# Kernel optimization log

Hardware: AMD Instinct MI355X
Metric: run time of the kernel (lower is better)

Reference implementation:

```python
import jax, jax.numpy as jnp
import numpy as np

# BigBird-roberta-base config with block_size=64, 12 layers
B = 1; S = 2048; D = 768; F = 3072; V = 50358
L = 12; H = 12; HD = 64; BS = 64; NB = S // BS; R = 3
NEG = -1.0e9
NKB = 5 + R           # global(2) + window(3) + random(3) key blocks per query block
NK = NKB * BS         # gathered keys per query block


def _block_map(nb, r, seed=0):
    """Static per-query-block key-block indices + dedup mask (first occurrence kept)."""
    rng = np.random.default_rng(seed)
    idx = np.zeros((nb, 5 + r), np.int32)
    dedup = np.ones((nb, 5 + r), np.float32)
    for i in range(nb):
        lst = [0, nb - 1, max(i - 1, 0), i, min(i + 1, nb - 1)]
        cand = np.setdiff1d(np.arange(nb), np.array(lst))
        lst += list(rng.choice(cand, r, replace=False))
        seen = set()
        for j, b in enumerate(lst):
            idx[i, j] = int(b)
            if b in seen:
                dedup[i, j] = 0.0
            seen.add(int(b))
    return idx, dedup

BLK_IDX, BLK_DEDUP = _block_map(NB, R)


def layer_norm(x, s, b):
    m = jnp.mean(x, axis=-1, keepdims=True)
    v = jnp.mean(jnp.square(x - m), axis=-1, keepdims=True)
    return (x - m) * jax.lax.rsqrt(v + 1e-12) * s + b


def bigbird_attn(x, wq, wk, wv, bq, bk, bv, wo, bo, key_mask):
    # x: [B,S,D]; key_mask: [B,S] float (1=keep)
    q = (x @ wq + bq).reshape(B, S, H, HD).transpose(0, 2, 1, 3)  # [B,H,S,HD]
    k = (x @ wk + bk).reshape(B, S, H, HD).transpose(0, 2, 1, 3)
    v = (x @ wv + bv).reshape(B, S, H, HD).transpose(0, 2, 1, 3)
    scale = 1.0 / np.sqrt(HD)
    qb = q.reshape(B, H, NB, BS, HD)
    kb = k.reshape(B, H, NB, BS, HD)
    vb = v.reshape(B, H, NB, BS, HD)
    # gather sparse key/value blocks: [B,H,NB,NKB,BS,HD] -> [B,H,NB,NK,HD]
    kg = kb[:, :, BLK_IDX].reshape(B, H, NB, NK, HD)
    vg = vb[:, :, BLK_IDX].reshape(B, H, NB, NK, HD)
    scores = jnp.einsum('bhnqd,bhnkd->bhnqk', qb, kg) * scale  # [B,H,NB,BS,NK]
    kmb = key_mask.reshape(B, NB, BS)[:, BLK_IDX]               # [B,NB,NKB,BS]
    m = (kmb * BLK_DEDUP[None, :, :, None]).reshape(B, 1, NB, 1, NK)
    probs = jax.nn.softmax(scores + (1.0 - m) * NEG, axis=-1)
    ctx = jnp.einsum('bhnqk,bhnkd->bhnqd', probs, vg)           # [B,H,NB,BS,HD]
    # global query blocks (first & last) attend densely to all keys
    qg = jnp.concatenate([qb[:, :, 0], qb[:, :, -1]], axis=2)   # [B,H,2*BS,HD]
    sg = jnp.einsum('bhqd,bhkd->bhqk', qg, k) * scale
    sg = sg + (1.0 - key_mask[:, None, None, :]) * NEG
    cg = jnp.einsum('bhqk,bhkd->bhqd', jax.nn.softmax(sg, axis=-1), v)
    ctx = ctx.at[:, :, 0].set(cg[:, :, :BS]).at[:, :, -1].set(cg[:, :, BS:])
    ctx = ctx.reshape(B, H, S, HD).transpose(0, 2, 1, 3).reshape(B, S, D)
    return ctx @ wo + bo


def setup_inputs() -> dict:
    key = jax.random.key(0)
    ks = jax.random.split(key, 16)
    p = lambda k, shape: jax.random.normal(k, shape, jnp.float32) * 0.02
    return {
        'input_ids': jax.random.randint(ks[0], (B, S), 0, V),
        'attention_mask': jnp.ones((B, S), jnp.int32),
        'token_type_ids': jnp.zeros((B, S), jnp.int32),
        'word_emb': p(ks[1], (V, D)),
        'pos_emb': p(ks[2], (S, D)),
        'type_emb': p(ks[3], (2, D)),
        'emb_ln_s': jnp.ones((D,)), 'emb_ln_b': jnp.zeros((D,)),
        'Wq': p(ks[4], (L, D, D)), 'Wk': p(ks[5], (L, D, D)), 'Wv': p(ks[6], (L, D, D)),
        'bq': jnp.zeros((L, D)), 'bk': jnp.zeros((L, D)), 'bv': jnp.zeros((L, D)),
        'Wo': p(ks[7], (L, D, D)), 'bo': jnp.zeros((L, D)),
        'ln1_s': jnp.ones((L, D)), 'ln1_b': jnp.zeros((L, D)),
        'W1': p(ks[8], (L, D, F)), 'b1': jnp.zeros((L, F)),
        'W2': p(ks[9], (L, F, D)), 'b2': jnp.zeros((L, D)),
        'ln2_s': jnp.ones((L, D)), 'ln2_b': jnp.zeros((L, D)),
        'fc_w': p(ks[10], (D, V)), 'fc_b': jnp.zeros((V,)),
    }


def reference(input_ids, attention_mask, token_type_ids, word_emb, pos_emb, type_emb,
              emb_ln_s, emb_ln_b, Wq, Wk, Wv, bq, bk, bv, Wo, bo, ln1_s, ln1_b,
              W1, b1, W2, b2, ln2_s, ln2_b, fc_w, fc_b):
    x = word_emb[input_ids] + pos_emb[None] + type_emb[token_type_ids]
    x = layer_norm(x, emb_ln_s, emb_ln_b)
    km = attention_mask.astype(x.dtype)
    for l in range(L):
        a = bigbird_attn(x, Wq[l], Wk[l], Wv[l], bq[l], bk[l], bv[l], Wo[l], bo[l], km)
        x = layer_norm(x + a, ln1_s[l], ln1_b[l])
        hdd = jax.nn.gelu(x @ W1[l] + b1[l])
        x = layer_norm(x + hdd @ W2[l] + b2[l], ln2_s[l], ln2_b[l])
    return x @ fc_w + fc_b  # logits [B,S,V]
```

## Files before the change

kernel.cpp:

```cpp
#include <hip/hip_runtime.h>
#include <hip/hip_bf16.h>


#define S_LEN 2048
#define DMODEL 768
#define FFDIM 3072
#define VOCAB 50358
#define VPAD  50432
#define NLAYER 12
#define NHEAD 12
#define NB 32
#define NKB 8
#define QKVN 2304

typedef __attribute__((ext_vector_type(8))) short bfrag8;
typedef __attribute__((ext_vector_type(8))) unsigned short us8;
typedef __attribute__((ext_vector_type(4))) float facc4;

__device__ __forceinline__ unsigned short f2bf(float f) {
  unsigned int u = __builtin_bit_cast(unsigned int, f);
  u += 0x7fffu + ((u >> 16) & 1u);
  return (unsigned short)(u >> 16);
}
__device__ __forceinline__ float bf2f(unsigned short h) {
  unsigned int u = ((unsigned int)h) << 16;
  return __builtin_bit_cast(float, u);
}

#define MFMA16(a, b, c) __builtin_amdgcn_mfma_f32_16x16x32_bf16((a), (b), (c), 0, 0, 0)
#define GLDS16(g, l) __builtin_amdgcn_global_load_lds( \
    (const __attribute__((address_space(1))) void*)(g), \
    (__attribute__((address_space(3))) void*)(l), 16, 0, 0)

struct Pcg {
  unsigned long long hi, lo, inc_hi, inc_lo;
  int has32; unsigned int buf32;
};

__device__ __forceinline__ void pcg_step(Pcg& p) {
  const unsigned long long MH = 0x2360ed051fc65da4ull;
  const unsigned long long ML = 0x4385df649fccf645ull;
  unsigned long long rl = p.lo * ML;
  unsigned long long rh = __umul64hi(p.lo, ML) + p.lo * MH + p.hi * ML;
  unsigned long long nl = rl + p.inc_lo;
  unsigned long long nh = rh + p.inc_hi + (nl < rl ? 1ull : 0ull);
  p.lo = nl; p.hi = nh;
}
__device__ __forceinline__ unsigned long long pcg_next64(Pcg& p) {
  pcg_step(p);
  unsigned int rot = (unsigned int)(p.hi >> 58);
  unsigned long long x = p.hi ^ p.lo;
  return (x >> rot) | (x << ((64u - rot) & 63u));
}
__device__ __forceinline__ unsigned int pcg_next32(Pcg& p) {
  if (p.has32) { p.has32 = 0; return p.buf32; }
  unsigned long long n = pcg_next64(p);
  p.has32 = 1; p.buf32 = (unsigned int)(n >> 32);
  return (unsigned int)n;
}
__device__ __forceinline__ unsigned int lemire32(Pcg& p, unsigned int rng) {
  unsigned int rng_excl = rng + 1u;
  unsigned long long m = (unsigned long long)pcg_next32(p) * (unsigned long long)rng_excl;
  unsigned int leftover = (unsigned int)m;
  if (leftover < rng_excl) {
    unsigned int threshold = (0xffffffffu - rng) % rng_excl;
    while (leftover < threshold) {
      m = (unsigned long long)pcg_next32(p) * (unsigned long long)rng_excl;
      leftover = (unsigned int)m;
    }
  }
  return (unsigned int)(m >> 32);
}

__global__ void blockmap_kernel(int* __restrict__ blk_idx, float* __restrict__ dedup) {
  if (threadIdx.x != 0 || blockIdx.x != 0) return;
  unsigned int pool[4];
  unsigned int hc = 0x43b0d7e5u;
  auto ss_hash = [&hc](unsigned int val) {
    val ^= hc; hc *= 0x931e8875u; val *= hc; val ^= val >> 16; return val;
  };
  auto ss_mix = [](unsigned int x, unsigned int y) {
    unsigned int r = 0xca01f9ddu * x - 0x4973f715u * y;
    r ^= r >> 16; return r;
  };
  for (int i = 0; i < 4; ++i) pool[i] = ss_hash(0u);
  for (int s = 0; s < 4; ++s)
    for (int d = 0; d < 4; ++d)
      if (s != d) pool[d] = ss_mix(pool[d], ss_hash(pool[s]));
  unsigned int st32[8];
  unsigned int hb = 0x8b51f9ddu;
  for (int i = 0; i < 8; ++i) {
    unsigned int dv = pool[i & 3];
    dv ^= hb; hb *= 0x58f38dedu; dv *= hb; dv ^= dv >> 16;
    st32[i] = dv;
  }
  unsigned long long sd[4];
  for (int i = 0; i < 4; ++i)
    sd[i] = (unsigned long long)st32[2*i] | ((unsigned long long)st32[2*i+1] << 32);
  Pcg p;
  p.inc_hi = (sd[2] << 1) | (sd[3] >> 63);
  p.inc_lo = (sd[3] << 1) | 1ull;
  p.hi = 0ull; p.lo = 0ull;
  pcg_step(p);
  unsigned long long ol = p.lo;
  p.lo = ol + sd[1];
  p.hi = p.hi + sd[0] + (p.lo < ol ? 1ull : 0ull);
  pcg_step(p);
  p.has32 = 0; p.buf32 = 0;

  for (int i = 0; i < NB; ++i) {
    int lst[8];
    lst[0] = 0; lst[1] = NB - 1;
    lst[2] = (i > 0) ? i - 1 : 0;
    lst[3] = i;
    lst[4] = (i + 1 < NB - 1) ? i + 1 : NB - 1;
    bool excl[NB];
    for (int c = 0; c < NB; ++c) excl[c] = false;
    for (int j = 0; j < 5; ++j) excl[lst[j]] = true;
    int cand[NB], n = 0;
    for (int c = 0; c < NB; ++c) if (!excl[c]) cand[n++] = c;
    long long idx[3];
    unsigned long long hs[4] = {~0ull, ~0ull, ~0ull, ~0ull};
    for (int tI = 0; tI < 3; ++tI) {
      unsigned long long j = (unsigned long long)(n - 3 + tI);
      unsigned long long val = (unsigned long long)lemire32(p, (unsigned int)j);
      unsigned long long loc = val & 3ull;
      while (hs[loc] != ~0ull && hs[loc] != val) loc = (loc + 1ull) & 3ull;
      if (hs[loc] == ~0ull) { hs[loc] = val; idx[tI] = (long long)val; }
      else {
        loc = j & 3ull;
        while (hs[loc] != ~0ull) loc = (loc + 1ull) & 3ull;
        hs[loc] = j; idx[tI] = (long long)j;
      }
    }
    for (int fi = 2; fi >= 1; --fi) {
      int fj = (int)lemire32(p, (unsigned int)fi);
      long long tmpv = idx[fi]; idx[fi] = idx[fj]; idx[fj] = tmpv;
    }
    lst[5] = cand[idx[0]]; lst[6] = cand[idx[1]]; lst[7] = cand[idx[2]];

    unsigned int seen = 0u;
    for (int j = 0; j < 8; ++j) {
      blk_idx[i*8 + j] = lst[j];
      dedup[i*8 + j] = ((seen >> lst[j]) & 1u) ? 0.0f : 1.0f;
      seen |= (1u << lst[j]);
    }
  }
}

__global__ __launch_bounds__(256) void tconv_kernel(
    const float* __restrict__ src, unsigned short* __restrict__ dst,
    int K, int N, size_t src_stride, size_t dst_stride) {
  __shared__ float tile[64][65];
  src += (size_t)blockIdx.z * src_stride;
  dst += (size_t)blockIdx.z * dst_stride;
  int n0 = blockIdx.x * 64, k0 = blockIdx.y * 64;
  int t = threadIdx.x;
  int tr = t >> 4, tc = (t & 15) * 4;
  if ((N & 3) == 0 && n0 + 64 <= N) {
    #pragma unroll
    for (int i = 0; i < 4; ++i) {
      int k = k0 + tr + i * 16;
      float4 v = *reinterpret_cast<const float4*>(src + (size_t)k * N + n0 + tc);
      tile[tr + i*16][tc + 0] = v.x; tile[tr + i*16][tc + 1] = v.y;
      tile[tr + i*16][tc + 2] = v.z; tile[tr + i*16][tc + 3] = v.w;
    }
  } else if ((N & 1) == 0 && n0 + 64 <= N) {
    #pragma unroll
    for (int i = 0; i < 4; ++i) {
      int k = k0 + tr + i * 16;
      float2 v0 = *reinterpret_cast<const float2*>(src + (size_t)k * N + n0 + tc);
      float2 v1 = *reinterpret_cast<const float2*>(src + (size_t)k * N + n0 + tc + 2);
      tile[tr + i*16][tc + 0] = v0.x; tile[tr + i*16][tc + 1] = v0.y;
      tile[tr + i*16][tc + 2] = v1.x; tile[tr + i*16][tc + 3] = v1.y;
    }
  } else {
    for (int i = 0; i < 4; ++i) {
      int k = k0 + tr + i * 16;
      #pragma unroll
      for (int q2 = 0; q2 < 4; ++q2) {
        int n = n0 + tc + q2;
        tile[tr + i*16][tc + q2] = (n < N) ? src[(size_t)k * N + n] : 0.0f;
      }
    }
  }
  __syncthreads();
  int wr_ = t >> 2, wc_ = (t & 3) * 16;
  us8 w0, w1;
  #pragma unroll
  for (int j = 0; j < 8; ++j) {
    w0[j] = f2bf(tile[wc_ + j][wr_]);
    w1[j] = f2bf(tile[wc_ + 8 + j][wr_]);
  }
  size_t b = (size_t)(n0 + wr_) * K + k0 + wc_;
  *reinterpret_cast<us8*>(dst + b) = w0;
  *reinterpret_cast<us8*>(dst + b + 8) = w1;
}

__global__ void bias_cat_kernel(const float* __restrict__ bq, const float* __restrict__ bk,
                                const float* __restrict__ bv, float* __restrict__ dst) {
  int l = blockIdx.x;
  for (int i = threadIdx.x; i < QKVN; i += blockDim.x) {
    float v = (i < 768) ? bq[l*768 + i] : (i < 1536) ? bk[l*768 + i - 768] : bv[l*768 + i - 1536];
    dst[l*QKVN + i] = v;
  }
}

__device__ __forceinline__ float block_sum256(float v, float* red) {
  for (int off = 32; off > 0; off >>= 1) v += __shfl_down(v, off);
  int wv = threadIdx.x >> 6;
  if ((threadIdx.x & 63) == 0) red[wv] = v;
  __syncthreads();
  float r = red[0] + red[1] + red[2] + red[3];
  __syncthreads();
  return r;
}

__global__ void embed_ln_kernel(const int* __restrict__ ids, const int* __restrict__ tts,
                                const float* __restrict__ we, const float* __restrict__ pe,
                                const float* __restrict__ te, const float* __restrict__ lns,
                                const float* __restrict__ lnb, float* __restrict__ x,
                                unsigned short* __restrict__ xh) {
  __shared__ float red[4];
  int row = blockIdx.x, t = threadIdx.x;
  int id = ids[row], ty = tts[row];
  float e[3]; float s = 0.0f;
  for (int j = 0; j < 3; ++j) {
    int d = t + 256*j;
    e[j] = we[(size_t)id*DMODEL + d] + pe[(size_t)row*DMODEL + d] + te[(size_t)ty*DMODEL + d];
    s += e[j];
  }
  float mean = block_sum256(s, red) * (1.0f/768.0f);
  float vs = 0.0f;
  for (int j = 0; j < 3; ++j) { float dd = e[j] - mean; vs += dd*dd; }
  float var = block_sum256(vs, red) * (1.0f/768.0f);
  float inv = rsqrtf(var + 1e-12f);
  for (int j = 0; j < 3; ++j) {
    int d = t + 256*j;
    float val = (e[j] - mean) * inv * lns[d] + lnb[d];
    size_t idx = (size_t)row*DMODEL + d;
    x[idx] = val;
    xh[idx] = f2bf(val);
  }
}

__global__ void resln_kernel(float* __restrict__ x, const float* __restrict__ a,
                             const float* __restrict__ lns, const float* __restrict__ lnb,
                             unsigned short* __restrict__ xh) {
  __shared__ float red[4];
  int row = blockIdx.x, t = threadIdx.x;
  float e[3]; float s = 0.0f;
  for (int j = 0; j < 3; ++j) {
    int d = t + 256*j;
    e[j] = x[(size_t)row*DMODEL + d] + a[(size_t)row*DMODEL + d];
    s += e[j];
  }
  float mean = block_sum256(s, red) * (1.0f/768.0f);
  float vs = 0.0f;
  for (int j = 0; j < 3; ++j) { float dd = e[j] - mean; vs += dd*dd; }
  float var = block_sum256(vs, red) * (1.0f/768.0f);
  float inv = rsqrtf(var + 1e-12f);
  for (int j = 0; j < 3; ++j) {
    int d = t + 256*j;
    float val = (e[j] - mean) * inv * lns[d] + lnb[d];
    size_t idx = (size_t)row*DMODEL + d;
    x[idx] = val;
    xh[idx] = f2bf(val);
  }
}

template<int TN, int OMODE, int ACT>
__global__ __launch_bounds__(256) void gemm9_kernel(
    const unsigned short* __restrict__ A_g, const unsigned short* __restrict__ Bt,
    const float* __restrict__ bias,
    float* __restrict__ Cf, unsigned short* __restrict__ Ch,
    int K, int Nreal) {
  __shared__ alignas(16) unsigned short As[3][128][32];
  __shared__ alignas(16) unsigned short Bs[3][TN][32];
  constexpr int NFR = (TN == 128) ? 4 : 2;
  constexpr int NLOADS = 2 + ((TN == 128) ? 2 : 1);
  int t = threadIdx.x;
  int m0 = (int)blockIdx.x * 128, n0 = (int)blockIdx.y * TN;

  int wave = t >> 6, lane = t & 63, l16 = lane & 15, lk = lane >> 4;
  int wr = wave >> 1, wc = wave & 1;
  int row16 = lane >> 2, seg4 = lane & 3;
  const int srcoff = (seg4 ^ ((row16 >> 1) & 3)) * 8;
  const int swzrd = (lk ^ ((l16 >> 1) & 3)) * 8;

  const unsigned short* ag = A_g + (size_t)(m0 + wave*32 + row16) * K + srcoff;
  const unsigned short* bg = Bt + (size_t)(n0 + (TN == 128 ? wave*32 : wave*16) + row16) * K + srcoff;
  const size_t K16 = (size_t)16 * K;

  auto STAGE = [&](int buf, int kit) {
    int k0 = kit << 5;
    GLDS16(ag + k0, &As[buf][wave*32][0]);
    GLDS16(ag + K16 + k0, &As[buf][wave*32 + 16][0]);
    if constexpr (TN == 128) {
      GLDS16(bg + k0, &Bs[buf][wave*32][0]);
      GLDS16(bg + K16 + k0, &Bs[buf][wave*32 + 16][0]);
    } else {
      GLDS16(bg + k0, &Bs[buf][wave*16][0]);
    }
  };

  facc4 acc[4][NFR];
  #pragma unroll
  for (int mi = 0; mi < 4; ++mi)
    #pragma unroll
    for (int ni = 0; ni < NFR; ++ni)
      acc[mi][ni] = (facc4){0.f, 0.f, 0.f, 0.f};

  const int nk = K >> 5;
  STAGE(0, 0);
  int cur = 0;
  for (int it = 0; it < nk; ++it) {
    int nxt = (cur == 2) ? 0 : cur + 1;
    if (it + 1 < nk) {
      STAGE(nxt, it + 1);
      asm volatile("s_waitcnt vmcnt(%0)" :: "n"(NLOADS) : "memory");
    } else {
      asm volatile("s_waitcnt vmcnt(0)" ::: "memory");
    }
    __builtin_amdgcn_sched_barrier(0);
    __builtin_amdgcn_s_barrier();
    __builtin_amdgcn_sched_barrier(0);
    bfrag8 af[4], bf[NFR];
    #pragma unroll
    for (int mi = 0; mi < 4; ++mi)
      af[mi] = *reinterpret_cast<const bfrag8*>(&As[cur][wr*64 + mi*16 + l16][swzrd]);
    #pragma unroll
    for (int ni = 0; ni < NFR; ++ni)
      bf[ni] = *reinterpret_cast<const bfrag8*>(&Bs[cur][(TN == 128 ? wc*64 : wc*32) + ni*16 + l16][swzrd]);
    #pragma unroll
    for (int mi = 0; mi < 4; ++mi)
      #pragma unroll
      for (int ni = 0; ni < NFR; ++ni)
        acc[mi][ni] = MFMA16(af[mi], bf[ni], acc[mi][ni]);
    cur = nxt;
  }

  #pragma unroll
  for (int mi = 0; mi < 4; ++mi)
    #pragma unroll
    for (int ni = 0; ni < NFR; ++ni) {
      int col = n0 + (TN == 128 ? wc*64 : wc*32) + ni*16 + l16;
      if (col >= Nreal) continue;
      float bv = bias[col];
      #pragma unroll
      for (int r2 = 0; r2 < 4; ++r2) {
        int row = m0 + wr*64 + mi*16 + lk*4 + r2;
        float val = acc[mi][ni][r2] + bv;
        if (ACT == 1) {
          float xx = val;
          val = 0.5f * xx * (1.0f + tanhf(0.7978845608028654f * (xx + 0.044715f * xx * xx * xx)));
        }
        size_t idx = (size_t)row * Nreal + col;
        if (OMODE == 0) Cf[idx] = val;
        else Ch[idx] = f2bf(val);
      }
    }
}

__device__ __forceinline__ void stage_glds64_swz(unsigned short (*dst)[64],
    const unsigned short* __restrict__ src, int ld, int t) {
  int w = t >> 6, lane = t & 63;
  int row8 = lane >> 3;
  int seg = (lane & 7) ^ (row8 & 7);
  const unsigned short* s = src + (size_t)(w*16 + row8) * ld + seg * 8;
  GLDS16(s, &dst[w*16][0]);
  GLDS16(s + (size_t)8 * ld, &dst[w*16 + 8][0]);
}

__device__ __forceinline__ void stage_T_pad(unsigned short (*dst)[66],
    const unsigned short* __restrict__ src, int ld, int t) {
  int row = t >> 2, colb = (t & 3) * 16;
  us8 h0 = *reinterpret_cast<const us8*>(src + (size_t)row*ld + colb);
  us8 h1 = *reinterpret_cast<const us8*>(src + (size_t)row*ld + colb + 8);
  #pragma unroll
  for (int j = 0; j < 8; ++j) {
    dst[colb + j][row] = h0[j];
    dst[colb + 8 + j][row] = h1[j];
  }
}

__global__ __launch_bounds__(256) void attn_kernel(
    const unsigned short* __restrict__ qkvh,
    const int* __restrict__ blk_idx, const float* __restrict__ dedup,
    const int* __restrict__ amask,
    unsigned short* __restrict__ ctxh,
    float* __restrict__ go, float* __restrict__ gm, float* __restrict__ gl) {
  __shared__ alignas(16) unsigned short Qs[64][64];
  __shared__ alignas(16) unsigned short KVs[64][64];
  __shared__ alignas(16) unsigned short Vs[64][66];
  __shared__ alignas(16) unsigned short Pt[64][68];
  int h = blockIdx.y;
  int bx = (int)blockIdx.x;
  const bool is_glob = (bx >= 30);
  int g = is_glob ? ((bx - 30) >> 2) : 0;
  int part = is_glob ? ((bx - 30) & 3) : 0;
  int qi = is_glob ? (g ? (NB - 1) : 0) : (bx + 1);
  int t = threadIdx.x, wave = t >> 6, lane = t & 63, l16 = lane & 15, lk = lane >> 4;
  const int swq0 = ((lk ^ (l16 & 7))) * 8;
  const int swq1 = (((4 + lk) ^ (l16 & 7))) * 8;

  stage_glds64_swz(Qs, qkvh + (size_t)(qi*64)*QKVN + h*64, QKVN, t);
  __syncthreads();
  const bfrag8 q0 = *reinterpret_cast<const bfrag8*>(&Qs[wave*16 + l16][swq0]);
  const bfrag8 q1 = *reinterpret_cast<const bfrag8*>(&Qs[wave*16 + l16][swq1]);

  float mrow[4] = {-3.0e38f, -3.0e38f, -3.0e38f, -3.0e38f};
  float lrow[4] = {0.f, 0.f, 0.f, 0.f};
  facc4 o[4];
  #pragma unroll
  for (int ni = 0; ni < 4; ++ni) o[ni] = (facc4){0.f, 0.f, 0.f, 0.f};

  for (int kb = 0; kb < 8; ++kb) {
    int b; float dd;
    if (is_glob) { b = part*8 + kb; dd = 1.0f; }
    else { b = blk_idx[qi*NKB + kb]; dd = dedup[qi*NKB + kb]; }
    __syncthreads();
    stage_glds64_swz(KVs, qkvh + (size_t)(b*64)*QKVN + DMODEL + h*64, QKVN, t);
    __syncthreads();
    float s[4][4];
    #pragma unroll
    for (int ni = 0; ni < 4; ++ni) {
      bfrag8 k0 = *reinterpret_cast<const bfrag8*>(&KVs[ni*16 + l16][swq0]);
      bfrag8 k1 = *reinterpret_cast<const bfrag8*>(&KVs[ni*16 + l16][swq1]);
      facc4 sa = (facc4){0.f, 0.f, 0.f, 0.f};
      sa = MFMA16(q0, k0, sa);
      sa = MFMA16(q1, k1, sa);
      int colk = ni*16 + l16;
      float mk = (float)amask[b*64 + colk] * dd;
      float addm = (1.0f - mk) * (-1.0e9f);
      #pragma unroll
      for (int r = 0; r < 4; ++r) s[ni][r] = sa[r] * 0.125f + addm;
    }
    float pexp[4][4];
    #pragma unroll
    for (int r = 0; r < 4; ++r) {
      float tm = fmaxf(fmaxf(s[0][r], s[1][r]), fmaxf(s[2][r], s[3][r]));
      tm = fmaxf(tm, __shfl_xor(tm, 1));
      tm = fmaxf(tm, __shfl_xor(tm, 2));
      tm = fmaxf(tm, __shfl_xor(tm, 4));
      tm = fmaxf(tm, __shfl_xor(tm, 8));
      float mn = fmaxf(mrow[r], tm);
      float f = expf(mrow[r] - mn);
      #pragma unroll
      for (int ni = 0; ni < 4; ++ni) o[ni][r] *= f;
      float ps = 0.0f;
      #pragma unroll
      for (int ni = 0; ni < 4; ++ni) { pexp[ni][r] = expf(s[ni][r] - mn); ps += pexp[ni][r]; }
      ps += __shfl_xor(ps, 1);
      ps += __shfl_xor(ps, 2);
      ps += __shfl_xor(ps, 4);
      ps += __shfl_xor(ps, 8);
      lrow[r] = lrow[r] * f + ps;
      mrow[r] = mn;
    }
    #pragma unroll
    for (int ni = 0; ni < 4; ++ni)
      #pragma unroll
      for (int r = 0; r < 4; ++r)
        Pt[wave*16 + lk*4 + r][ni*16 + l16] = f2bf(pexp[ni][r]);
    stage_T_pad(Vs, qkvh + (size_t)(b*64)*QKVN + 2*DMODEL + h*64, QKVN, t);
    __syncthreads();
    #pragma unroll
    for (int kc = 0; kc < 2; ++kc) {
      bfrag8 ph = *reinterpret_cast<const bfrag8*>(&Pt[wave*16 + l16][kc*32 + lk*8]);
      #pragma unroll
      for (int ni = 0; ni < 4; ++ni) {
        bfrag8 vh = *reinterpret_cast<const bfrag8*>(&Vs[ni*16 + l16][kc*32 + lk*8]);
        o[ni] = MFMA16(ph, vh, o[ni]);
      }
    }
  }

  if (!is_glob) {
    float invl[4];
    #pragma unroll
    for (int r = 0; r < 4; ++r) invl[r] = 1.0f / lrow[r];
    #pragma unroll
    for (int ni = 0; ni < 4; ++ni)
      #pragma unroll
      for (int r = 0; r < 4; ++r) {
        int row = qi*64 + wave*16 + lk*4 + r;
        int col = h*64 + ni*16 + l16;
        ctxh[(size_t)row*DMODEL + col] = f2bf(o[ni][r] * invl[r]);
      }
  } else {
    int pidx = (g * NHEAD + h) * 4 + part;
    float* gob = go + (size_t)pidx * 64 * 64;
    #pragma unroll
    for (int ni = 0; ni < 4; ++ni)
      #pragma unroll
      for (int r = 0; r < 4; ++r)
        gob[(wave*16 + lk*4 + r) * 64 + ni*16 + l16] = o[ni][r];
    if (l16 == 0) {
      #pragma unroll
      for (int r = 0; r < 4; ++r) {
        int row = wave*16 + lk*4 + r;
        gm[pidx*64 + row] = mrow[r];
        gl[pidx*64 + row] = lrow[r];
      }
    }
  }
}

__global__ __launch_bounds__(256) void gattn_comb_kernel(
    const float* __restrict__ go, const float* __restrict__ gm,
    const float* __restrict__ gl, unsigned short* __restrict__ ctxh) {
  int g = blockIdx.x, h = blockIdx.y;
  int t = threadIdx.x;
  int row = t >> 2, cseg = (t & 3) * 16;
  int base = (g * NHEAD + h) * 4;
  float m = -3.0e38f;
  for (int p = 0; p < 4; ++p) m = fmaxf(m, gm[(base + p)*64 + row]);
  float w[4]; float l = 0.0f;
  for (int p = 0; p < 4; ++p) {
    w[p] = expf(gm[(base + p)*64 + row] - m);
    l += gl[(base + p)*64 + row] * w[p];
  }
  float inv = 1.0f / l;
  int qrow = (g ? (NB - 1) * 64 : 0) + row;
  for (int c = 0; c < 16; ++c) {
    float acc = 0.0f;
    for (int p = 0; p < 4; ++p)
      acc += go[((size_t)(base + p)*64 + row)*64 + cseg + c] * w[p];
    ctxh[(size_t)qrow*DMODEL + h*64 + cseg + c] = f2bf(acc * inv);
  }
}

extern "C" void kernel_launch(void* const* d_in, const int* in_sizes, int n_in,
                              void* d_out, int out_size, void* d_ws, size_t ws_size,
                              hipStream_t stream) {
  const int*   input_ids  = (const int*)d_in[0];
  const int*   attn_mask  = (const int*)d_in[1];
  const int*   token_type = (const int*)d_in[2];
  const float* word_emb   = (const float*)d_in[3];
  const float* pos_emb    = (const float*)d_in[4];
  const float* type_emb   = (const float*)d_in[5];
  const float* emb_ln_s   = (const float*)d_in[6];
  const float* emb_ln_b   = (const float*)d_in[7];
  const float* Wq = (const float*)d_in[8];
  const float* Wk = (const float*)d_in[9];
  const float* Wv = (const float*)d_in[10];
  const float* bq = (const float*)d_in[11];
  const float* bk = (const float*)d_in[12];
  const float* bv = (const float*)d_in[13];
  const float* Wo = (const float*)d_in[14];
  const float* bo = (const float*)d_in[15];
  const float* ln1_s = (const float*)d_in[16];
  const float* ln1_b = (const float*)d_in[17];
  const float* W1 = (const float*)d_in[18];
  const float* b1 = (const float*)d_in[19];
  const float* W2 = (const float*)d_in[20];
  const float* b2 = (const float*)d_in[21];
  const float* ln2_s = (const float*)d_in[22];
  const float* ln2_b = (const float*)d_in[23];
  const float* fc_w = (const float*)d_in[24];
  const float* fc_b = (const float*)d_in[25];
  float* out = (float*)d_out;

  unsigned char* base = (unsigned char*)d_ws;
  size_t off = 0;
  auto carve = [&](size_t bytes) -> void* {
    void* p = base + off;
    off = (off + bytes + 255) & ~(size_t)255;
    return p;
  };
  int*   blk_i = (int*)carve(256 * 4);
  float* dedup = (float*)carve(256 * 4);
  float* bqkv  = (float*)carve((size_t)NLAYER * QKVN * 4);
  float* x     = (float*)carve((size_t)S_LEN * DMODEL * 4);
  float* tmp   = (float*)carve((size_t)S_LEN * DMODEL * 4);
  unsigned short* xh   = (unsigned short*)carve((size_t)S_LEN * DMODEL * 2);
  unsigned short* qkvh = (unsigned short*)carve((size_t)S_LEN * QKVN * 2);
  unsigned short* ctxh = (unsigned short*)carve((size_t)S_LEN * DMODEL * 2);
  unsigned short* hbh  = (unsigned short*)carve((size_t)S_LEN * FFDIM * 2);
  float* go    = (float*)carve((size_t)2 * NHEAD * 4 * 64 * 64 * 4);
  float* gm    = (float*)carve((size_t)2 * NHEAD * 4 * 64 * 4);
  float* gl    = (float*)carve((size_t)2 * NHEAD * 4 * 64 * 4);
  unsigned short* qkvT = (unsigned short*)carve((size_t)NLAYER * QKVN * DMODEL * 2);
  unsigned short* woT  = (unsigned short*)carve((size_t)NLAYER * DMODEL * DMODEL * 2);
  unsigned short* w1T  = (unsigned short*)carve((size_t)NLAYER * FFDIM * DMODEL * 2);
  unsigned short* w2T  = (unsigned short*)carve((size_t)NLAYER * DMODEL * FFDIM * 2);
  unsigned short* fcT  = (unsigned short*)carve((size_t)VPAD * DMODEL * 2);

  blockmap_kernel<<<1, 1, 0, stream>>>(blk_i, dedup);

  const size_t DD = (size_t)DMODEL * DMODEL;
  dim3 g768(12, 12, NLAYER);
  tconv_kernel<<<g768, 256, 0, stream>>>(Wq, qkvT + 0,            DMODEL, DMODEL, DD, (size_t)QKVN * DMODEL);
  tconv_kernel<<<g768, 256, 0, stream>>>(Wk, qkvT + 768 * DMODEL, DMODEL, DMODEL, DD, (size_t)QKVN * DMODEL);
  tconv_kernel<<<g768, 256, 0, stream>>>(Wv, qkvT + 1536 * DMODEL,DMODEL, DMODEL, DD, (size_t)QKVN * DMODEL);
  tconv_kernel<<<g768, 256, 0, stream>>>(Wo, woT, DMODEL, DMODEL, DD, DD);
  tconv_kernel<<<dim3(48, 12, NLAYER), 256, 0, stream>>>(W1, w1T, DMODEL, FFDIM, (size_t)DMODEL * FFDIM, (size_t)FFDIM * DMODEL);
  tconv_kernel<<<dim3(12, 48, NLAYER), 256, 0, stream>>>(W2, w2T, FFDIM, DMODEL, (size_t)FFDIM * DMODEL, (size_t)DMODEL * FFDIM);
  tconv_kernel<<<dim3(VPAD / 64, 12, 1), 256, 0, stream>>>(fc_w, fcT, DMODEL, VOCAB, 0, 0);
  bias_cat_kernel<<<NLAYER, 256, 0, stream>>>(bq, bk, bv, bqkv);

  embed_ln_kernel<<<S_LEN, 256, 0, stream>>>(input_ids, token_type, word_emb, pos_emb,
                                             type_emb, emb_ln_s, emb_ln_b, x, xh);

  for (int l = 0; l < NLAYER; ++l) {
    gemm9_kernel<128, 2, 0><<<dim3(16, QKVN/128), 256, 0, stream>>>(
        xh, qkvT + (size_t)l * QKVN * DMODEL, bqkv + (size_t)l * QKVN,
        nullptr, qkvh, DMODEL, QKVN);

    attn_kernel<<<dim3(38, NHEAD), 256, 0, stream>>>(
        qkvh, blk_i, dedup, attn_mask, ctxh, go, gm, gl);
    gattn_comb_kernel<<<dim3(2, NHEAD), 256, 0, stream>>>(go, gm, gl, ctxh);

    gemm9_kernel<64, 0, 0><<<dim3(16, DMODEL/64), 256, 0, stream>>>(
        ctxh, woT + (size_t)l * DD, bo + (size_t)l * DMODEL,
        tmp, nullptr, DMODEL, DMODEL);
    resln_kernel<<<S_LEN, 256, 0, stream>>>(x, tmp, ln1_s + l*DMODEL, ln1_b + l*DMODEL, xh);

    gemm9_kernel<128, 2, 1><<<dim3(16, FFDIM/128), 256, 0, stream>>>(
        xh, w1T + (size_t)l * FFDIM * DMODEL, b1 + (size_t)l * FFDIM,
        nullptr, hbh, DMODEL, FFDIM);
    gemm9_kernel<64, 0, 0><<<dim3(16, DMODEL/64), 256, 0, stream>>>(
        hbh, w2T + (size_t)l * DMODEL * FFDIM, b2 + (size_t)l * DMODEL,
        tmp, nullptr, FFDIM, DMODEL);
    resln_kernel<<<S_LEN, 256, 0, stream>>>(x, tmp, ln2_s + l*DMODEL, ln2_b + l*DMODEL, xh);
  }

  gemm9_kernel<128, 0, 0><<<dim3(16, VPAD/128), 256, 0, stream>>>(
      xh, fcT, fc_b, out, nullptr, DMODEL, VOCAB);
}
```

Before: 2.647 ms.

## Swizzle GEMM workgroups across XCDs and prefetch V loads in attention

Remaps GEMM workgroup IDs so that tiles processed on the same XCD are contiguous in M, improving L2 reuse of shared operand tiles. In the attention kernel, V rows are loaded into registers while the K tile is being staged, replacing a separate load-then-transpose step. Explicit barriers and waitcnts replace syncthreads to allow this overlap. The remap assumes the block count is divisible by 8, and the manual waitcnt handling is fragile.

```diff
diff --git a/kernel.cpp b/kernel.cpp
--- a/kernel.cpp
+++ b/kernel.cpp
@@ -270,7 +270,7 @@
 }
 
 template<int TN, int OMODE, int ACT>
-__global__ __launch_bounds__(256) void gemm9_kernel(
+__global__ __launch_bounds__(256) void gemm10_kernel(
     const unsigned short* __restrict__ A_g, const unsigned short* __restrict__ Bt,
     const float* __restrict__ bias,
     float* __restrict__ Cf, unsigned short* __restrict__ Ch,
@@ -280,7 +280,12 @@
   constexpr int NFR = (TN == 128) ? 4 : 2;
   constexpr int NLOADS = 2 + ((TN == 128) ? 2 : 1);
   int t = threadIdx.x;
-  int m0 = (int)blockIdx.x * 128, n0 = (int)blockIdx.y * TN;
+  int mb = (int)gridDim.x;
+  int nwg = mb * (int)gridDim.y;
+  int lin = (int)blockIdx.x + mb * (int)blockIdx.y;
+  int cpx = nwg >> 3;
+  int nl = (lin & 7) * cpx + (lin >> 3);
+  int m0 = (nl % mb) * 128, n0 = (nl / mb) * TN;
 
   int wave = t >> 6, lane = t & 63, l16 = lane & 15, lk = lane >> 4;
   int wr = wave >> 1, wc = wave & 1;
@@ -370,18 +375,6 @@
   const unsigned short* s = src + (size_t)(w*16 + row8) * ld + seg * 8;
   GLDS16(s, &dst[w*16][0]);
   GLDS16(s + (size_t)8 * ld, &dst[w*16 + 8][0]);
-}
-
-__device__ __forceinline__ void stage_T_pad(unsigned short (*dst)[66],
-    const unsigned short* __restrict__ src, int ld, int t) {
-  int row = t >> 2, colb = (t & 3) * 16;
-  us8 h0 = *reinterpret_cast<const us8*>(src + (size_t)row*ld + colb);
-  us8 h1 = *reinterpret_cast<const us8*>(src + (size_t)row*ld + colb + 8);
-  #pragma unroll
-  for (int j = 0; j < 8; ++j) {
-    dst[colb + j][row] = h0[j];
-    dst[colb + 8 + j][row] = h1[j];
-  }
 }
 
 __global__ __launch_bounds__(256) void attn_kernel(
@@ -403,6 +396,7 @@
   int t = threadIdx.x, wave = t >> 6, lane = t & 63, l16 = lane & 15, lk = lane >> 4;
   const int swq0 = ((lk ^ (l16 & 7))) * 8;
   const int swq1 = (((4 + lk) ^ (l16 & 7))) * 8;
+  const int vrow = t >> 2, vcolb = (t & 3) * 16;
 
   stage_glds64_swz(Qs, qkvh + (size_t)(qi*64)*QKVN + h*64, QKVN, t);
   __syncthreads();
@@ -419,9 +413,15 @@
     int b; float dd;
     if (is_glob) { b = part*8 + kb; dd = 1.0f; }
     else { b = blk_idx[qi*NKB + kb]; dd = dedup[qi*NKB + kb]; }
-    __syncthreads();
+    __builtin_amdgcn_s_barrier();
     stage_glds64_swz(KVs, qkvh + (size_t)(b*64)*QKVN + DMODEL + h*64, QKVN, t);
-    __syncthreads();
+    __builtin_amdgcn_sched_barrier(0);
+    const unsigned short* vsrc = qkvh + (size_t)(b*64 + vrow)*QKVN + 2*DMODEL + h*64 + vcolb;
+    us8 v0 = *reinterpret_cast<const us8*>(vsrc);
+    us8 v1 = *reinterpret_cast<const us8*>(vsrc + 8);
+    asm volatile("s_waitcnt vmcnt(2)" ::: "memory");
+    __builtin_amdgcn_sched_barrier(0);
+    __builtin_amdgcn_s_barrier();
     float s[4][4];
     #pragma unroll
     for (int ni = 0; ni < 4; ++ni) {
@@ -463,8 +463,14 @@
       #pragma unroll
       for (int r = 0; r < 4; ++r)
         Pt[wave*16 + lk*4 + r][ni*16 + l16] = f2bf(pexp[ni][r]);
-    stage_T_pad(Vs, qkvh + (size_t)(b*64)*QKVN + 2*DMODEL + h*64, QKVN, t);
-    __syncthreads();
+    #pragma unroll
+    for (int j = 0; j < 8; ++j) {
+      Vs[vcolb + j][vrow] = v0[j];
+      Vs[vcolb + 8 + j][vrow] = v1[j];
+    }
+    asm volatile("s_waitcnt lgkmcnt(0)" ::: "memory");
+    __builtin_amdgcn_sched_barrier(0);
+    __builtin_amdgcn_s_barrier();
     #pragma unroll
     for (int kc = 0; kc < 2; ++kc) {
       bfrag8 ph = *reinterpret_cast<const bfrag8*>(&Pt[wave*16 + l16][kc*32 + lk*8]);
@@ -604,7 +610,7 @@
                                              type_emb, emb_ln_s, emb_ln_b, x, xh);
 
   for (int l = 0; l < NLAYER; ++l) {
-    gemm9_kernel<128, 2, 0><<<dim3(16, QKVN/128), 256, 0, stream>>>(
+    gemm10_kernel<128, 2, 0><<<dim3(16, QKVN/128), 256, 0, stream>>>(
         xh, qkvT + (size_t)l * QKVN * DMODEL, bqkv + (size_t)l * QKVN,
         nullptr, qkvh, DMODEL, QKVN);
 
@@ -612,20 +618,20 @@
         qkvh, blk_i, dedup, attn_mask, ctxh, go, gm, gl);
     gattn_comb_kernel<<<dim3(2, NHEAD), 256, 0, stream>>>(go, gm, gl, ctxh);
 
-    gemm9_kernel<64, 0, 0><<<dim3(16, DMODEL/64), 256, 0, stream>>>(
+    gemm10_kernel<64, 0, 0><<<dim3(16, DMODEL/64), 256, 0, stream>>>(
         ctxh, woT + (size_t)l * DD, bo + (size_t)l * DMODEL,
         tmp, nullptr, DMODEL, DMODEL);
     resln_kernel<<<S_LEN, 256, 0, stream>>>(x, tmp, ln1_s + l*DMODEL, ln1_b + l*DMODEL, xh);
 
-    gemm9_kernel<128, 2, 1><<<dim3(16, FFDIM/128), 256, 0, stream>>>(
+    gemm10_kernel<128, 2, 1><<<dim3(16, FFDIM/128), 256, 0, stream>>>(
         xh, w1T + (size_t)l * FFDIM * DMODEL, b1 + (size_t)l * FFDIM,
         nullptr, hbh, DMODEL, FFDIM);
-    gemm9_kernel<64, 0, 0><<<dim3(16, DMODEL/64), 256, 0, stream>>>(
+    gemm10_kernel<64, 0, 0><<<dim3(16, DMODEL/64), 256, 0, stream>>>(
         hbh, w2T + (size_t)l * DMODEL * FFDIM, b2 + (size_t)l * DMODEL,
         tmp, nullptr, FFDIM, DMODEL);
     resln_kernel<<<S_LEN, 256, 0, stream>>>(x, tmp, ln2_s + l*DMODEL, ln2_b + l*DMODEL, xh);
   }
 
-  gemm9_kernel<128, 0, 0><<<dim3(16, VPAD/128), 256, 0, stream>>>(
+  gemm10_kernel<128, 0, 0><<<dim3(16, VPAD/128), 256, 0, stream>>>(
       xh, fcT, fc_b, out, nullptr, DMODEL, VOCAB);
 }
```

Result: faster. 2.592 ms (-2.1%).
